# Kernel optimization log

Measured on AMD Instinct MI355X. Metric: run time of the kernel, lower is better.

Reference implementation:

```python
import jax, jax.numpy as jnp
import numpy as np

RADIUS = 50.0
EPS = 1e-8


def setup_inputs() -> dict:
    key = jax.random.key(0)
    k1, k2, k3, k4, k5 = jax.random.split(key, 5)
    N, E, H = 16384, 524288, 256
    x = jax.random.normal(k1, (N, H), dtype=jnp.float32)
    edge_index = jax.random.randint(k2, (2, E), 0, N, dtype=jnp.int32)
    spatial_coords = jax.random.uniform(k3, (N, 2), dtype=jnp.float32) * 1000.0
    w1 = jax.random.normal(k4, (3, H // 2), dtype=jnp.float32) * 0.02
    b1 = jnp.zeros((H // 2,), dtype=jnp.float32)
    w2 = jax.random.normal(k5, (H // 2, H), dtype=jnp.float32) * 0.02
    b2 = jnp.zeros((H,), dtype=jnp.float32)
    return {"x": x, "edge_index": edge_index, "spatial_coords": spatial_coords,
            "w1": w1, "b1": b1, "w2": w2, "b2": b2}


def reference(x, edge_index, spatial_coords, w1, b1, w2, b2):
    N = x.shape[0]
    row, col = edge_index[0], edge_index[1]

    # degree via scatter-add (segment_sum)
    ones = jnp.ones(row.shape, dtype=x.dtype)
    degree = jax.ops.segment_sum(ones, row, num_segments=N)  # [N]

    # spatial density: count neighbors within RADIUS (full pairwise, vectorized)
    sq = jnp.sum(spatial_coords * spatial_coords, axis=-1)  # [N]
    d2 = sq[:, None] + sq[None, :] - 2.0 * (spatial_coords @ spatial_coords.T)  # [N,N] squared dists
    in_radius = (d2 <= RADIUS * RADIUS).astype(x.dtype)
    density = jnp.sum(in_radius, axis=1) - 1.0  # exclude self
    density = density / (jnp.max(density) + EPS)

    # local feature variance: || x - mean(neighbor features) ||
    nbr_sum = jax.ops.segment_sum(x[col], row, num_segments=N)  # [N,H]
    cnt = jnp.clip(degree, 1.0)[:, None]
    nbr_mean = nbr_sum / cnt
    fvar = jnp.linalg.norm(x - nbr_mean, axis=-1)  # [N]
    fvar = fvar / (jnp.max(fvar) + EPS)

    feats = jnp.stack([degree / (jnp.max(degree) + EPS), density, fvar], axis=-1)  # [N,3]
    h = jax.nn.relu(feats @ w1 + b1)
    return h @ w2 + b2  # [N, hidden_dim]
```

## Files before the change

kernel.cpp:

```cpp
#include <hip/hip_runtime.h>
#include <math.h>

#define R2 2500.0f
#define EPSF 1e-8f

constexpr int H   = 256;
constexpr int HH  = 128;
constexpr int NB  = 8;
constexpr int BSH = 11;
constexpr int RPW = 4;

__global__ void __launch_bounds__(256) k_degcell(
    const int* __restrict__ row, const int* __restrict__ col,
    int* __restrict__ deg4, const float* __restrict__ coords,
    int* __restrict__ cellcnt, int EB4, int N) {
    if ((int)blockIdx.x < EB4) {
        int e4 = blockIdx.x * 256 + threadIdx.x;
        int4 r = ((const int4*)row)[e4];
        int4 c = ((const int4*)col)[e4];
        atomicAdd(&deg4[r.x * NB + (c.x >> BSH)], 1);
        atomicAdd(&deg4[r.y * NB + (c.y >> BSH)], 1);
        atomicAdd(&deg4[r.z * NB + (c.z >> BSH)], 1);
        atomicAdd(&deg4[r.w * NB + (c.w >> BSH)], 1);
    } else {
        int t2 = ((int)blockIdx.x - EB4) * 256 + threadIdx.x;
        float4 cc = ((const float4*)coords)[t2];
        int cx0 = (int)(cc.x * 0.02f); if (cx0 > 19) cx0 = 19;
        int cy0 = (int)(cc.y * 0.02f); if (cy0 > 19) cy0 = 19;
        int cx1 = (int)(cc.z * 0.02f); if (cx1 > 19) cx1 = 19;
        int cy1 = (int)(cc.w * 0.02f); if (cy1 > 19) cy1 = 19;
        atomicAdd(&cellcnt[cy0 * 20 + cx0], 1);
        atomicAdd(&cellcnt[cy1 * 20 + cx1], 1);
    }
}

__global__ void __launch_bounds__(256) k_bsum(const int* __restrict__ deg4,
                                              int* __restrict__ bsum) {
    int t = threadIdx.x;
    int4 v = ((const int4*)deg4)[blockIdx.x * 256 + t];
    int sum = v.x + v.y + v.z + v.w;
#pragma unroll
    for (int off = 32; off > 0; off >>= 1) sum += __shfl_xor(sum, off, 64);
    __shared__ int sw[4];
    if ((t & 63) == 0) sw[t >> 6] = sum;
    __syncthreads();
    if (t == 0) bsum[blockIdx.x] = sw[0] + sw[1] + sw[2] + sw[3];
}

__global__ void __launch_bounds__(512) k_scatcell(
    const int* __restrict__ deg4, const int* __restrict__ bsum,
    int* __restrict__ rp4, int* __restrict__ cur4, int M,
    const int* __restrict__ cellcnt, int* __restrict__ cellstart,
    int* __restrict__ cellcur) {
    __shared__ int s[512];
    int t = threadIdx.x;
    int blk = blockIdx.x;
    if (blk < gridDim.x - 1) {
        s[t] = (t < 128) ? bsum[t] : 0;
        __syncthreads();
        for (int off = 1; off < 128; off <<= 1) {
            int v = (t < 128) ? s[t] : 0;
            int add = (t >= off && t < 128) ? s[t - off] : 0;
            __syncthreads();
            if (t < 128) s[t] = v + add;
            __syncthreads();
        }
        int boff = (blk > 0) ? s[blk - 1] : 0;
        if (t < 256) {
            int lane = t & 63, w = t >> 6;
            int4 v = ((const int4*)deg4)[blk * 256 + t];
            int tsum = v.x + v.y + v.z + v.w;
            int incl = tsum;
#pragma unroll
            for (int off = 1; off < 64; off <<= 1) {
                int n = __shfl_up(incl, off, 64);
                if (lane >= off) incl += n;
            }
            __shared__ int wsum[4];
            if (lane == 63) wsum[w] = incl;
            __syncthreads();
            int woff = 0;
#pragma unroll
            for (int k = 0; k < 4; k++) woff += (k < w) ? wsum[k] : 0;
            int excl = boff + woff + (incl - tsum);
            int4 r;
            r.x = excl;
            r.y = excl + v.x;
            r.z = excl + v.x + v.y;
            r.w = excl + v.x + v.y + v.z;
            ((int4*)rp4)[blk * 256 + t]  = r;
            ((int4*)cur4)[blk * 256 + t] = r;
            if (blk == 127 && t == 255) rp4[M] = excl + tsum;
        }
    } else {
        s[t] = (t < 400) ? cellcnt[t] : 0;
        __syncthreads();
        for (int off = 1; off < 512; off <<= 1) {
            int v = s[t];
            int add = (t >= off) ? s[t - off] : 0;
            __syncthreads();
            s[t] = v + add;
            __syncthreads();
        }
        if (t < 400) {
            int excl = (t > 0) ? s[t - 1] : 0;
            cellstart[t] = excl;
            cellcur[t]   = excl;
        }
        if (t == 400) cellstart[400] = s[399];
    }
}

__global__ void __launch_bounds__(256) k_fillcell(
    const int* __restrict__ row, const int* __restrict__ col,
    int* __restrict__ cur4, int* __restrict__ cols,
    const float* __restrict__ coords, int* __restrict__ cellcur,
    float4* __restrict__ pts, int EB4, int N) {
    if ((int)blockIdx.x < EB4) {
        int e4 = blockIdx.x * 256 + threadIdx.x;
        int4 r = ((const int4*)row)[e4];
        int4 c = ((const int4*)col)[e4];
        int p0 = atomicAdd(&cur4[r.x * NB + (c.x >> BSH)], 1); cols[p0] = c.x;
        int p1 = atomicAdd(&cur4[r.y * NB + (c.y >> BSH)], 1); cols[p1] = c.y;
        int p2 = atomicAdd(&cur4[r.z * NB + (c.z >> BSH)], 1); cols[p2] = c.z;
        int p3 = atomicAdd(&cur4[r.w * NB + (c.w >> BSH)], 1); cols[p3] = c.w;
    } else {
        int t2 = ((int)blockIdx.x - EB4) * 256 + threadIdx.x;
        float4 cc = ((const float4*)coords)[t2];
        int i0 = t2 * 2;
        int cx0 = (int)(cc.x * 0.02f); if (cx0 > 19) cx0 = 19;
        int cy0 = (int)(cc.y * 0.02f); if (cy0 > 19) cy0 = 19;
        int p0 = atomicAdd(&cellcur[cy0 * 20 + cx0], 1);
        pts[p0] = make_float4(cc.x, cc.y, cc.x * cc.x + cc.y * cc.y,
                              __int_as_float(i0));
        int cx1 = (int)(cc.z * 0.02f); if (cx1 > 19) cx1 = 19;
        int cy1 = (int)(cc.w * 0.02f); if (cy1 > 19) cy1 = 19;
        int p1 = atomicAdd(&cellcur[cy1 * 20 + cx1], 1);
        pts[p1] = make_float4(cc.z, cc.w, cc.z * cc.z + cc.w * cc.w,
                              __int_as_float(i0 + 1));
    }
}

__global__ void __launch_bounds__(256, 8) k_fvar_dgrid(
    const float* __restrict__ x, const int* __restrict__ rp4,
    const int* __restrict__ cols, float* __restrict__ fvar,
    const float4* __restrict__ pts, const int* __restrict__ cellstart,
    int* __restrict__ dens, int FBk, int N) {
    int wave = threadIdx.x >> 6;
    int lane = threadIdx.x & 63;
    if ((int)blockIdx.x < FBk) {
        int i0 = (blockIdx.x * 4 + wave) * RPW;
        const float4* xb = (const float4*)x;

        int bnd = rp4[i0 * NB + (lane < 4 * NB ? lane : 4 * NB)];

        float4 acc0 = make_float4(0.f, 0.f, 0.f, 0.f);
        float4 acc1 = make_float4(0.f, 0.f, 0.f, 0.f);
        float4 acc2 = make_float4(0.f, 0.f, 0.f, 0.f);
        float4 acc3 = make_float4(0.f, 0.f, 0.f, 0.f);

        for (int b = 0; b < NB; b++) {
#pragma unroll
            for (int r = 0; r < RPW; r++) {
                float4& a = (r == 0) ? acc0 : (r == 1) ? acc1
                          : (r == 2) ? acc2 : acc3;
                int s = __shfl(bnd, r * NB + b, 64);
                int e = __shfl(bnd, r * NB + b + 1, 64);
                if (e <= s) continue;
                for (int p0 = s; p0 < e; p0 += 64) {
                    int m = e - p0; if (m > 64) m = 64;
                    int idx = cols[p0 + (lane < m ? lane : m - 1)];
                    for (int j = 0; j < m; j += 8) {
                        int nb2 = m - j; if (nb2 > 8) nb2 = 8;
                        size_t o0 = (size_t)__shfl(idx, j + 0, 64) * 64 + lane;
                        size_t o1 = (1 < nb2) ? (size_t)__shfl(idx, j + 1, 64) * 64 + lane : 0;
                        size_t o2 = (2 < nb2) ? (size_t)__shfl(idx, j + 2, 64) * 64 + lane : 0;
                        size_t o3 = (3 < nb2) ? (size_t)__shfl(idx, j + 3, 64) * 64 + lane : 0;
                        size_t o4 = (4 < nb2) ? (size_t)__shfl(idx, j + 4, 64) * 64 + lane : 0;
                        size_t o5 = (5 < nb2) ? (size_t)__shfl(idx, j + 5, 64) * 64 + lane : 0;
                        size_t o6 = (6 < nb2) ? (size_t)__shfl(idx, j + 6, 64) * 64 + lane : 0;
                        size_t o7 = (7 < nb2) ? (size_t)__shfl(idx, j + 7, 64) * 64 + lane : 0;
                        float4 g0 = xb[o0];
                        float4 g1 = xb[o1];
                        float4 g2 = xb[o2];
                        float4 g3 = xb[o3];
                        float4 g4 = xb[o4];
                        float4 g5 = xb[o5];
                        float4 g6 = xb[o6];
                        float4 g7 = xb[o7];
                        float w1 = (1 < nb2) ? 1.0f : 0.0f;
                        float w2 = (2 < nb2) ? 1.0f : 0.0f;
                        float w3 = (3 < nb2) ? 1.0f : 0.0f;
                        float w4 = (4 < nb2) ? 1.0f : 0.0f;
                        float w5 = (5 < nb2) ? 1.0f : 0.0f;
                        float w6 = (6 < nb2) ? 1.0f : 0.0f;
                        float w7 = (7 < nb2) ? 1.0f : 0.0f;
                        a.x += g0.x; a.y += g0.y; a.z += g0.z; a.w += g0.w;
                        a.x = fmaf(g1.x, w1, a.x); a.y = fmaf(g1.y, w1, a.y);
                        a.z = fmaf(g1.z, w1, a.z); a.w = fmaf(g1.w, w1, a.w);
                        a.x = fmaf(g2.x, w2, a.x); a.y = fmaf(g2.y, w2, a.y);
                        a.z = fmaf(g2.z, w2, a.z); a.w = fmaf(g2.w, w2, a.w);
                        a.x = fmaf(g3.x, w3, a.x); a.y = fmaf(g3.y, w3, a.y);
                        a.z = fmaf(g3.z, w3, a.z); a.w = fmaf(g3.w, w3, a.w);
                        a.x = fmaf(g4.x, w4, a.x); a.y = fmaf(g4.y, w4, a.y);
                        a.z = fmaf(g4.z, w4, a.z); a.w = fmaf(g4.w, w4, a.w);
                        a.x = fmaf(g5.x, w5, a.x); a.y = fmaf(g5.y, w5, a.y);
                        a.z = fmaf(g5.z, w5, a.z); a.w = fmaf(g5.w, w5, a.w);
                        a.x = fmaf(g6.x, w6, a.x); a.y = fmaf(g6.y, w6, a.y);
                        a.z = fmaf(g6.z, w6, a.z); a.w = fmaf(g6.w, w6, a.w);
                        a.x = fmaf(g7.x, w7, a.x); a.y = fmaf(g7.y, w7, a.y);
                        a.z = fmaf(g7.z, w7, a.z); a.w = fmaf(g7.w, w7, a.w);
                    }
                }
            }
        }

#define FIN(RR, ACCR)                                                   \
        {                                                               \
            int i = i0 + (RR);                                          \
            float cnt = fmaxf((float)(__shfl(bnd, (RR) * NB + NB, 64) - \
                                      __shfl(bnd, (RR) * NB, 64)), 1.0f); \
            float4 xi = xb[(size_t)i * 64 + lane];                      \
            float dx = xi.x - ACCR.x / cnt;                             \
            float dy = xi.y - ACCR.y / cnt;                             \
            float dz = xi.z - ACCR.z / cnt;                             \
            float dw = xi.w - ACCR.w / cnt;                             \
            float ss = dx * dx + dy * dy + dz * dz + dw * dw;           \
            _Pragma("unroll")                                           \
            for (int off = 32; off > 0; off >>= 1) ss += __shfl_xor(ss, off, 64); \
            if (lane == 0) fvar[i] = sqrtf(ss);                         \
        }

        FIN(0, acc0);
        FIN(1, acc1);
        FIN(2, acc2);
        FIN(3, acc3);
#undef FIN
    } else {
        int t = ((int)blockIdx.x - FBk) * 4 + wave;
        float4 p = pts[t];
        int cx = (int)(p.x * 0.02f); if (cx > 19) cx = 19;
        int cy = (int)(p.y * 0.02f); if (cy > 19) cy = 19;
        int x0 = cx - 2; if (x0 < 0) x0 = 0;
        int x1 = cx + 2; if (x1 > 19) x1 = 19;
        int y0 = cy - 2; if (y0 < 0) y0 = 0;
        int y1 = cy + 2; if (y1 > 19) y1 = 19;
        int cnt = 0;
        for (int yy = y0; yy <= y1; yy++) {
            int rowb = yy * 20;
            int s = cellstart[rowb + x0];
            int e = cellstart[rowb + x1 + 1];
            for (int q = s + lane; q < e; q += 64) {
                float4 pq = pts[q];
                float dot = p.x * pq.x + p.y * pq.y;
                float d2 = (p.z + pq.z) - 2.0f * dot;
                cnt += (d2 <= R2) ? 1 : 0;
            }
        }
#pragma unroll
        for (int off = 32; off > 0; off >>= 1) cnt += __shfl_xor(cnt, off, 64);
        if (lane == 0) dens[__float_as_int(p.w)] = cnt;
    }
}

__global__ void __launch_bounds__(256) k_scal(
    const int* __restrict__ rp4, const int* __restrict__ dens,
    const float* __restrict__ fvar, int* __restrict__ scal, int N) {
    __shared__ int sd[4], sn[4];
    __shared__ float sf[4];
    int t = threadIdx.x;
    int g = blockIdx.x * 256 + t;
    int stride = 256 * gridDim.x;
    int md = 0, mn = 0;
    float mf = 0.f;
    for (int i = g; i < N; i += stride) {
        md = max(md, rp4[(i + 1) * NB] - rp4[i * NB]);
        mn = max(mn, dens[i]);
        mf = fmaxf(mf, fvar[i]);
    }
#pragma unroll
    for (int off = 32; off > 0; off >>= 1) {
        md = max(md, __shfl_xor(md, off, 64));
        mn = max(mn, __shfl_xor(mn, off, 64));
        mf = fmaxf(mf, __shfl_xor(mf, off, 64));
    }
    int w = t >> 6, l = t & 63;
    if (l == 0) { sd[w] = md; sn[w] = mn; sf[w] = mf; }
    __syncthreads();
    if (t == 0) {
#pragma unroll
        for (int k = 1; k < 4; k++) {
            md = max(md, sd[k]);
            mn = max(mn, sn[k]);
            mf = fmaxf(mf, sf[k]);
        }
        atomicMax(&scal[0], md);
        atomicMax(&scal[1], mn);
        atomicMax(&scal[2], __float_as_int(mf));
    }
}

__global__ void __launch_bounds__(256) k_mlp(
    const float* __restrict__ w1, const float* __restrict__ b1,
    const float* __restrict__ w2, const float* __restrict__ b2,
    const int* __restrict__ rp4, const int* __restrict__ dens,
    const float* __restrict__ fvar, const int* __restrict__ scal,
    float* __restrict__ out, int N) {
    __shared__ float sh_h[HH];
    int j = threadIdx.x;
    float wv[HH];
#pragma unroll
    for (int l = 0; l < HH; l++) wv[l] = w2[l * H + j];
    float bj = b2[j];
    float maxdeg  = (float)scal[0] + EPSF;
    float maxdens = (float)(scal[1] - 1) + EPSF;
    float maxfv   = __int_as_float(scal[2]) + EPSF;
    float w1a = 0.f, w1b = 0.f, w1c = 0.f, b1j = 0.f;
    if (j < HH) { w1a = w1[j]; w1b = w1[HH + j]; w1c = w1[2 * HH + j]; b1j = b1[j]; }
    for (int i = blockIdx.x; i < N; i += gridDim.x) {
        float f0 = (float)(rp4[(i + 1) * NB] - rp4[i * NB]) / maxdeg;
        float f1 = (float)(dens[i] - 1) / maxdens;
        float f2 = fvar[i] / maxfv;
        if (j < HH) {
            float h = f0 * w1a + f1 * w1b + f2 * w1c + b1j;
            sh_h[j] = fmaxf(h, 0.0f);
        }
        __syncthreads();
        float acc = bj;
#pragma unroll
        for (int l = 0; l < HH; l++) acc = fmaf(sh_h[l], wv[l], acc);
        out[(size_t)i * H + j] = acc;
        __syncthreads();
    }
}

extern "C" void kernel_launch(void* const* d_in, const int* in_sizes, int n_in,
                              void* d_out, int out_size, void* d_ws, size_t ws_size,
                              hipStream_t stream) {
    const float* x      = (const float*)d_in[0];
    const int*   ei     = (const int*)d_in[1];
    const float* coords = (const float*)d_in[2];
    const float* w1     = (const float*)d_in[3];
    const float* b1     = (const float*)d_in[4];
    const float* w2     = (const float*)d_in[5];
    const float* b2     = (const float*)d_in[6];
    float* out = (float*)d_out;

    const int N = in_sizes[2] / 2;
    const int E = in_sizes[1] / 2;
    const int M = N * NB;
    const int NBLK = M / 1024;
    const int EB4 = E / 1024;
    const int CB2 = N / 512;
    const int FBk = N / (4 * RPW);
    const int DB  = N / 4;
    const int* row = ei;
    const int* col = ei + E;

    int* ws        = (int*)d_ws;
    int* scal      = ws;
    int* deg4      = ws + 4;
    int* cellcnt   = ws + 4 + M;
    int* rp4       = ws + 408 + M;
    int* cur4      = rp4 + M + 4;
    int* cellstart = cur4 + M;
    int* cellcur   = cellstart + 404;
    int* dens_cnt  = cellcur + 400;
    float* fvarp   = (float*)(dens_cnt + N);
    int* bsum      = dens_cnt + 2 * N;
    int* boff      = bsum + 128;
    int* cols      = boff + 128;
    float4* pts    = (float4*)(cols + E);

    hipMemsetAsync(ws, 0, (size_t)(408 + M) * sizeof(int), stream);

    k_degcell<<<EB4 + CB2, 256, 0, stream>>>(row, col, deg4, coords, cellcnt,
                                             EB4, N);
    k_bsum<<<NBLK, 256, 0, stream>>>(deg4, bsum);
    k_scatcell<<<NBLK + 1, 512, 0, stream>>>(deg4, bsum, rp4, cur4, M,
                                             cellcnt, cellstart, cellcur);
    k_fillcell<<<EB4 + CB2, 256, 0, stream>>>(row, col, cur4, cols,
                                              coords, cellcur, pts, EB4, N);

    k_fvar_dgrid<<<FBk + DB, 256, 0, stream>>>(x, rp4, cols, fvarp,
                                               pts, cellstart, dens_cnt, FBk, N);

    k_scal<<<64, 256, 0, stream>>>(rp4, dens_cnt, fvarp, scal, N);

    k_mlp<<<1024, 256, 0, stream>>>(w1, b1, w2, b2, rp4, dens_cnt, fvarp, scal,
                                    out, N);
}
```

Measured before the change: 262.2 us.

## Fuse max-reduction into MLP kernel and simplify fvar gather loop

Drops the separate k_scal kernel. Each of the 1024 MLP blocks now recomputes the global maxima of degree, density and fvar over all N nodes before running its MLP rows. This removes a kernel launch and the atomic round-trip, at the cost of every block redundantly reading about 3N values. The fvar gather also drops the per-slot index guards and the empty-range early exit, and the launch bound minimum occupancy is lowered from 8 to 4 blocks per CU to give the compiler more registers.

```diff
diff --git a/kernel.cpp b/kernel.cpp
--- a/kernel.cpp
+++ b/kernel.cpp
@@ -141,7 +141,7 @@
     }
 }
 
-__global__ void __launch_bounds__(256, 8) k_fvar_dgrid(
+__global__ void __launch_bounds__(256, 4) k_fvar_dgrid(
     const float* __restrict__ x, const int* __restrict__ rp4,
     const int* __restrict__ cols, float* __restrict__ fvar,
     const float4* __restrict__ pts, const int* __restrict__ cellstart,
@@ -151,8 +151,7 @@
     if ((int)blockIdx.x < FBk) {
         int i0 = (blockIdx.x * 4 + wave) * RPW;
         const float4* xb = (const float4*)x;
-
-        int bnd = rp4[i0 * NB + (lane < 4 * NB ? lane : 4 * NB)];
+        int bnd = rp4[i0 * NB + (lane < 32 ? lane : 32)];
 
         float4 acc0 = make_float4(0.f, 0.f, 0.f, 0.f);
         float4 acc1 = make_float4(0.f, 0.f, 0.f, 0.f);
@@ -166,28 +165,19 @@
                           : (r == 2) ? acc2 : acc3;
                 int s = __shfl(bnd, r * NB + b, 64);
                 int e = __shfl(bnd, r * NB + b + 1, 64);
-                if (e <= s) continue;
                 for (int p0 = s; p0 < e; p0 += 64) {
                     int m = e - p0; if (m > 64) m = 64;
                     int idx = cols[p0 + (lane < m ? lane : m - 1)];
                     for (int j = 0; j < m; j += 8) {
                         int nb2 = m - j; if (nb2 > 8) nb2 = 8;
-                        size_t o0 = (size_t)__shfl(idx, j + 0, 64) * 64 + lane;
-                        size_t o1 = (1 < nb2) ? (size_t)__shfl(idx, j + 1, 64) * 64 + lane : 0;
-                        size_t o2 = (2 < nb2) ? (size_t)__shfl(idx, j + 2, 64) * 64 + lane : 0;
-                        size_t o3 = (3 < nb2) ? (size_t)__shfl(idx, j + 3, 64) * 64 + lane : 0;
-                        size_t o4 = (4 < nb2) ? (size_t)__shfl(idx, j + 4, 64) * 64 + lane : 0;
-                        size_t o5 = (5 < nb2) ? (size_t)__shfl(idx, j + 5, 64) * 64 + lane : 0;
-                        size_t o6 = (6 < nb2) ? (size_t)__shfl(idx, j + 6, 64) * 64 + lane : 0;
-                        size_t o7 = (7 < nb2) ? (size_t)__shfl(idx, j + 7, 64) * 64 + lane : 0;
-                        float4 g0 = xb[o0];
-                        float4 g1 = xb[o1];
-                        float4 g2 = xb[o2];
-                        float4 g3 = xb[o3];
-                        float4 g4 = xb[o4];
-                        float4 g5 = xb[o5];
-                        float4 g6 = xb[o6];
-                        float4 g7 = xb[o7];
+                        float4 g0 = xb[(size_t)__shfl(idx, j + 0, 64) * 64 + lane];
+                        float4 g1 = xb[(size_t)__shfl(idx, j + 1, 64) * 64 + lane];
+                        float4 g2 = xb[(size_t)__shfl(idx, j + 2, 64) * 64 + lane];
+                        float4 g3 = xb[(size_t)__shfl(idx, j + 3, 64) * 64 + lane];
+                        float4 g4 = xb[(size_t)__shfl(idx, j + 4, 64) * 64 + lane];
+                        float4 g5 = xb[(size_t)__shfl(idx, j + 5, 64) * 64 + lane];
+                        float4 g6 = xb[(size_t)__shfl(idx, j + 6, 64) * 64 + lane];
+                        float4 g7 = xb[(size_t)__shfl(idx, j + 7, 64) * 64 + lane];
                         float w1 = (1 < nb2) ? 1.0f : 0.0f;
                         float w2 = (2 < nb2) ? 1.0f : 0.0f;
                         float w3 = (3 < nb2) ? 1.0f : 0.0f;
@@ -263,17 +253,20 @@
     }
 }
 
-__global__ void __launch_bounds__(256) k_scal(
+__global__ void __launch_bounds__(256) k_mlp(
+    const float* __restrict__ w1, const float* __restrict__ b1,
+    const float* __restrict__ w2, const float* __restrict__ b2,
     const int* __restrict__ rp4, const int* __restrict__ dens,
-    const float* __restrict__ fvar, int* __restrict__ scal, int N) {
-    __shared__ int sd[4], sn[4];
-    __shared__ float sf[4];
-    int t = threadIdx.x;
-    int g = blockIdx.x * 256 + t;
-    int stride = 256 * gridDim.x;
+    const float* __restrict__ fvar, float* __restrict__ out, int N) {
+    __shared__ float sh_h[HH];
+    __shared__ int smd[4], smn[4];
+    __shared__ float smf[4];
+    int j = threadIdx.x;
+    int wv_ = j >> 6, ln = j & 63;
+
     int md = 0, mn = 0;
     float mf = 0.f;
-    for (int i = g; i < N; i += stride) {
+    for (int i = j; i < N; i += 256) {
         md = max(md, rp4[(i + 1) * NB] - rp4[i * NB]);
         mn = max(mn, dens[i]);
         mf = fmaxf(mf, fvar[i]);
@@ -284,37 +277,19 @@
         mn = max(mn, __shfl_xor(mn, off, 64));
         mf = fmaxf(mf, __shfl_xor(mf, off, 64));
     }
-    int w = t >> 6, l = t & 63;
-    if (l == 0) { sd[w] = md; sn[w] = mn; sf[w] = mf; }
+    if (ln == 0) { smd[wv_] = md; smn[wv_] = mn; smf[wv_] = mf; }
     __syncthreads();
-    if (t == 0) {
-#pragma unroll
-        for (int k = 1; k < 4; k++) {
-            md = max(md, sd[k]);
-            mn = max(mn, sn[k]);
-            mf = fmaxf(mf, sf[k]);
-        }
-        atomicMax(&scal[0], md);
-        atomicMax(&scal[1], mn);
-        atomicMax(&scal[2], __float_as_int(mf));
-    }
-}
-
-__global__ void __launch_bounds__(256) k_mlp(
-    const float* __restrict__ w1, const float* __restrict__ b1,
-    const float* __restrict__ w2, const float* __restrict__ b2,
-    const int* __restrict__ rp4, const int* __restrict__ dens,
-    const float* __restrict__ fvar, const int* __restrict__ scal,
-    float* __restrict__ out, int N) {
-    __shared__ float sh_h[HH];
-    int j = threadIdx.x;
+    md = max(max(smd[0], smd[1]), max(smd[2], smd[3]));
+    mn = max(max(smn[0], smn[1]), max(smn[2], smn[3]));
+    mf = fmaxf(fmaxf(smf[0], smf[1]), fmaxf(smf[2], smf[3]));
+    float maxdeg  = (float)md + EPSF;
+    float maxdens = (float)(mn - 1) + EPSF;
+    float maxfv   = mf + EPSF;
+
     float wv[HH];
 #pragma unroll
     for (int l = 0; l < HH; l++) wv[l] = w2[l * H + j];
     float bj = b2[j];
-    float maxdeg  = (float)scal[0] + EPSF;
-    float maxdens = (float)(scal[1] - 1) + EPSF;
-    float maxfv   = __int_as_float(scal[2]) + EPSF;
     float w1a = 0.f, w1b = 0.f, w1c = 0.f, b1j = 0.f;
     if (j < HH) { w1a = w1[j]; w1b = w1[HH + j]; w1c = w1[2 * HH + j]; b1j = b1[j]; }
     for (int i = blockIdx.x; i < N; i += gridDim.x) {
@@ -371,6 +346,7 @@
     int* boff      = bsum + 128;
     int* cols      = boff + 128;
     float4* pts    = (float4*)(cols + E);
+    (void)scal;
 
     hipMemsetAsync(ws, 0, (size_t)(408 + M) * sizeof(int), stream);
 
@@ -385,8 +361,6 @@
     k_fvar_dgrid<<<FBk + DB, 256, 0, stream>>>(x, rp4, cols, fvarp,
                                                pts, cellstart, dens_cnt, FBk, N);
 
-    k_scal<<<64, 256, 0, stream>>>(rp4, dens_cnt, fvarp, scal, N);
-
-    k_mlp<<<1024, 256, 0, stream>>>(w1, b1, w2, b2, rp4, dens_cnt, fvarp, scal,
+    k_mlp<<<1024, 256, 0, stream>>>(w1, b1, w2, b2, rp4, dens_cnt, fvarp,
                                     out, N);
 }
```

After: 286.8 us. 1.09x slower.
